# Kernel tuning notes

Hardware: AMD Instinct MI355X
Metric: run time of the kernel (lower is better)

Reference implementation:

```python
import jax, jax.numpy as jnp
import numpy as np

B, S, D, H = 4, 1024, 1024, 16
HD = D // H  # head_dim = 64
NEG = -1e9  # stands in for float('-inf') in masked_fill; numerically safe


def setup_inputs() -> dict:
    key = jax.random.key(0)
    ks = jax.random.split(key, 8)
    q = jax.random.normal(ks[0], (B, S, D), dtype=jnp.float32)
    k = jax.random.normal(ks[1], (B, S, D), dtype=jnp.float32)
    v = jax.random.normal(ks[2], (B, S, D), dtype=jnp.float32)
    # padding mask: True marks padded positions; pad out the tail of each sequence
    pos = jnp.arange(S)
    lengths = jnp.array([S, S - 64, S - 128, S - 256])
    padding_mask = pos[None, :] >= lengths[:, None]  # [B, S] bool
    # additive causal mask: 0 on/below diagonal, NEG above
    causal_mask = jnp.where(jnp.tril(jnp.ones((S, S), dtype=bool)), 0.0, NEG).astype(jnp.float32)
    scale = 1.0 / np.sqrt(D)
    Wq = jax.random.normal(ks[3], (D, D), dtype=jnp.float32) * scale
    Wk = jax.random.normal(ks[4], (D, D), dtype=jnp.float32) * scale
    Wv = jax.random.normal(ks[5], (D, D), dtype=jnp.float32) * scale
    Wo = jax.random.normal(ks[6], (D, D), dtype=jnp.float32) * scale
    return {"q": q, "k": k, "v": v, "padding_mask": padding_mask,
            "causal_mask": causal_mask, "Wq": Wq, "Wk": Wk, "Wv": Wv,
            "Wo": Wo, "n_heads": H}


def reference(q, k, v, padding_mask, causal_mask, Wq, Wk, Wv, Wo, n_heads):
    b, s, d = q.shape
    hd = d // n_heads
    # projections (nn.Linear: x @ W^T, no bias)
    qp = (q @ Wq.T).reshape(b, s, n_heads, hd).transpose(0, 2, 1, 3)  # [b,h,s,hd]
    kp = (k @ Wk.T).reshape(b, s, n_heads, hd).transpose(0, 2, 1, 3)
    vp = (v @ Wv.T).reshape(b, s, n_heads, hd).transpose(0, 2, 1, 3)
    scores = jnp.einsum('bhqd,bhkd->bhqk', qp, kp) / jnp.sqrt(jnp.float32(hd))
    # masked_fill(padding_mask, -inf): mask broadcast over heads and query dim
    scores = jnp.where(padding_mask[:, None, None, :], NEG, scores)
    scores = scores + causal_mask  # additive causal mask
    attn = jax.nn.softmax(scores, axis=-1)
    out = jnp.einsum('bhqk,bhkd->bhqd', attn, vp)
    out = out.transpose(0, 2, 1, 3).reshape(b, s, d)
    return out @ Wo.T
```

## Files before the change

### kernel.cpp

```cpp
#include <hip/hip_runtime.h>
#include <hip/hip_bf16.h>

#define BB 4
#define SS 1024
#define DD 1024
#define HH 16
#define HD 64
#define MM (BB*SS)


typedef __bf16 bf16x8 __attribute__((ext_vector_type(8)));
typedef __bf16 bf16x4 __attribute__((ext_vector_type(4)));
typedef float  f32x4  __attribute__((ext_vector_type(4)));

__global__ __launch_bounds__(256) void expand_mask(const void* __restrict__ pmraw,
                                                   float* __restrict__ madd,
                                                   int n)
{
    const unsigned char* bytes = (const unsigned char*)pmraw;
    __shared__ int isbool;
    if (threadIdx.x == 0) isbool = 0;
    __syncthreads();
    int flag = 0;
    for (int idx = threadIdx.x; idx < n; idx += 256) {
        if ((idx & 3) && bytes[idx]) flag = 1;
    }
    if (flag) atomicOr(&isbool, 1);
    __syncthreads();
    int i = blockIdx.x * 256 + threadIdx.x;
    if (i < n) {
        int v = isbool ? (int)bytes[i] : ((const int*)pmraw)[i];
        madd[i] = (v != 0) ? -1e9f : 0.0f;
    }
}

__global__ __launch_bounds__(256) void conv3(const float* __restrict__ s0,
                                             const float* __restrict__ s1,
                                             const float* __restrict__ s2,
                                             __bf16* __restrict__ d0,
                                             __bf16* __restrict__ d1,
                                             __bf16* __restrict__ d2)
{
    const float* s; __bf16* d;
    if (blockIdx.y == 0)      { s = s0; d = d0; }
    else if (blockIdx.y == 1) { s = s1; d = d1; }
    else                      { s = s2; d = d2; }
    int i = (blockIdx.x * 256 + threadIdx.x) * 4;
    float4 x = *(const float4*)(s + i);
    bf16x4 o;
    o[0] = (__bf16)x.x; o[1] = (__bf16)x.y;
    o[2] = (__bf16)x.z; o[3] = (__bf16)x.w;
    *(bf16x4*)(d + i) = o;
}

__global__ __launch_bounds__(256) void conv4(const float* __restrict__ s0,
                                             const float* __restrict__ s1,
                                             const float* __restrict__ s2,
                                             const float* __restrict__ s3,
                                             __bf16* __restrict__ d0,
                                             __bf16* __restrict__ d1,
                                             __bf16* __restrict__ d2,
                                             __bf16* __restrict__ d3)
{
    const float* s; __bf16* d;
    if (blockIdx.y == 0)      { s = s0; d = d0; }
    else if (blockIdx.y == 1) { s = s1; d = d1; }
    else if (blockIdx.y == 2) { s = s2; d = d2; }
    else                      { s = s3; d = d3; }
    int i = (blockIdx.x * 256 + threadIdx.x) * 4;
    float4 x = *(const float4*)(s + i);
    bf16x4 o;
    o[0] = (__bf16)x.x; o[1] = (__bf16)x.y;
    o[2] = (__bf16)x.z; o[3] = (__bf16)x.w;
    *(bf16x4*)(d + i) = o;
}

#define GM 128
#define GN 64
#define GK 64

__global__ __launch_bounds__(256) void gemm_qkv(const __bf16* __restrict__ qb,
                                                const __bf16* __restrict__ kb,
                                                const __bf16* __restrict__ vb,
                                                const __bf16* __restrict__ Wqb,
                                                const __bf16* __restrict__ Wkb,
                                                const __bf16* __restrict__ Wvb,
                                                __bf16* __restrict__ Qp,
                                                __bf16* __restrict__ Kp,
                                                __bf16* __restrict__ VpT)
{
    __shared__ __align__(16) __bf16 As[GM][GK];
    __shared__ __align__(16) __bf16 Bs[GN][GK];

    const __bf16 *A, *W; __bf16* C;
    const int z = blockIdx.z;
    if (z == 0)      { A = qb; W = Wqb; C = Qp;  }
    else if (z == 1) { A = kb; W = Wkb; C = Kp;  }
    else             { A = vb; W = Wvb; C = VpT; }

    const int tid  = threadIdx.x;
    const int lane = tid & 63;
    const int w    = tid >> 6;
    const int l15  = lane & 15;
    const int quad = lane >> 4;
    const int wr   = w >> 1;
    const int wc   = w & 1;

    const int m0 = blockIdx.y * GM;
    const int n0 = blockIdx.x * GN;

    const int srow = tid >> 3;
    const int scol = (tid & 7) * 8;

    const __bf16* gA = A + (size_t)(m0 + srow) * DD + scol;
    const __bf16* gB = W + (size_t)(n0 + srow) * DD + scol;

    f32x4 acc[4][2] = {};

    for (int k0 = 0; k0 < DD; k0 += GK) {
        __syncthreads();
        #pragma unroll
        for (int c = 0; c < 4; ++c)
            __builtin_amdgcn_global_load_lds(
                (const __attribute__((address_space(1))) void*)(gA + (size_t)c * 32 * DD + k0),
                (__attribute__((address_space(3))) void*)(&As[c * 32 + srow][scol]), 16, 0, 0);
        #pragma unroll
        for (int c = 0; c < 2; ++c)
            __builtin_amdgcn_global_load_lds(
                (const __attribute__((address_space(1))) void*)(gB + (size_t)c * 32 * DD + k0),
                (__attribute__((address_space(3))) void*)(&Bs[c * 32 + srow][scol]), 16, 0, 0);
        __syncthreads();

        #pragma unroll
        for (int ks = 0; ks < 2; ++ks) {
            bf16x8 af[4], bf[2];
            #pragma unroll
            for (int mt = 0; mt < 4; ++mt)
                af[mt] = *(const bf16x8*)&As[wr * 64 + mt * 16 + l15][ks * 32 + quad * 8];
            #pragma unroll
            for (int nt = 0; nt < 2; ++nt)
                bf[nt] = *(const bf16x8*)&Bs[wc * 32 + nt * 16 + l15][ks * 32 + quad * 8];
            #pragma unroll
            for (int mt = 0; mt < 4; ++mt)
                #pragma unroll
                for (int nt = 0; nt < 2; ++nt)
                    acc[mt][nt] = __builtin_amdgcn_mfma_f32_16x16x32_bf16(
                        af[mt], bf[nt], acc[mt][nt], 0, 0, 0);
        }
    }

    if (z == 0) {
        #pragma unroll
        for (int mt = 0; mt < 4; ++mt)
            #pragma unroll
            for (int nt = 0; nt < 2; ++nt)
                #pragma unroll
                for (int r = 0; r < 4; ++r)
                    acc[mt][nt][r] *= 0.125f;
    }

    if (z == 2) {
        #pragma unroll
        for (int mt = 0; mt < 4; ++mt)
            #pragma unroll
            for (int nt = 0; nt < 2; ++nt) {
                bf16x4 o;
                #pragma unroll
                for (int r = 0; r < 4; ++r) o[r] = (__bf16)acc[mt][nt][r];
                const int n = n0 + wc * 32 + nt * 16 + l15;
                const int m = m0 + wr * 64 + mt * 16 + quad * 4;
                *(bf16x4*)&C[(size_t)n * MM + m] = o;
            }
    } else {
        #pragma unroll
        for (int mt = 0; mt < 4; ++mt)
            #pragma unroll
            for (int nt = 0; nt < 2; ++nt)
                #pragma unroll
                for (int r = 0; r < 4; ++r)
                    C[(size_t)(m0 + wr * 64 + mt * 16 + quad * 4 + r) * DD +
                      (n0 + wc * 32 + nt * 16 + l15)] = (__bf16)acc[mt][nt][r];
    }
}

__global__ __launch_bounds__(256) void gemm_wo(const __bf16* __restrict__ A,
                                               const __bf16* __restrict__ W,
                                               float* __restrict__ C)
{
    __shared__ __align__(16) __bf16 As[64][64];
    __shared__ __align__(16) __bf16 Bs[64][64];

    const int tid  = threadIdx.x;
    const int lane = tid & 63;
    const int w    = tid >> 6;
    const int l15  = lane & 15;
    const int quad = lane >> 4;
    const int wr   = w >> 1;
    const int wc   = w & 1;

    const int m0 = blockIdx.y * 64;
    const int n0 = blockIdx.x * 64;

    const int srow = tid >> 3;
    const int scol = (tid & 7) * 8;

    const __bf16* gA = A + (size_t)(m0 + srow) * DD + scol;
    const __bf16* gB = W + (size_t)(n0 + srow) * DD + scol;

    f32x4 acc[2][2] = {};

    for (int k0 = 0; k0 < DD; k0 += 64) {
        __syncthreads();
        #pragma unroll
        for (int c = 0; c < 2; ++c)
            __builtin_amdgcn_global_load_lds(
                (const __attribute__((address_space(1))) void*)(gA + (size_t)c * 32 * DD + k0),
                (__attribute__((address_space(3))) void*)(&As[c * 32 + srow][scol]), 16, 0, 0);
        #pragma unroll
        for (int c = 0; c < 2; ++c)
            __builtin_amdgcn_global_load_lds(
                (const __attribute__((address_space(1))) void*)(gB + (size_t)c * 32 * DD + k0),
                (__attribute__((address_space(3))) void*)(&Bs[c * 32 + srow][scol]), 16, 0, 0);
        __syncthreads();

        #pragma unroll
        for (int ks = 0; ks < 2; ++ks) {
            bf16x8 af[2], bf[2];
            #pragma unroll
            for (int mt = 0; mt < 2; ++mt)
                af[mt] = *(const bf16x8*)&As[wr * 32 + mt * 16 + l15][ks * 32 + quad * 8];
            #pragma unroll
            for (int nt = 0; nt < 2; ++nt)
                bf[nt] = *(const bf16x8*)&Bs[wc * 32 + nt * 16 + l15][ks * 32 + quad * 8];
            #pragma unroll
            for (int mt = 0; mt < 2; ++mt)
                #pragma unroll
                for (int nt = 0; nt < 2; ++nt)
                    acc[mt][nt] = __builtin_amdgcn_mfma_f32_16x16x32_bf16(
                        af[mt], bf[nt], acc[mt][nt], 0, 0, 0);
        }
    }

    #pragma unroll
    for (int mt = 0; mt < 2; ++mt)
        #pragma unroll
        for (int nt = 0; nt < 2; ++nt)
            #pragma unroll
            for (int r = 0; r < 4; ++r)
                C[(size_t)(m0 + wr * 32 + mt * 16 + quad * 4 + r) * DD +
                  (n0 + wc * 32 + nt * 16 + l15)] = acc[mt][nt][r];
}

#define PSTRIDE 72

__global__ __launch_bounds__(256) void flash_attn(const __bf16* __restrict__ Qp,
                                                  const __bf16* __restrict__ Kp,
                                                  const __bf16* __restrict__ VpT,
                                                  const float* __restrict__ maskadd,
                                                  __bf16* __restrict__ Op)
{
    __shared__ __bf16 Pl[4][16][PSTRIDE];
    __shared__ float  Obuf[2][16][68];

    const int tid  = threadIdx.x;
    const int lane = tid & 63;
    const int w    = tid >> 6;
    const int l15  = lane & 15;
    const int quad = lane >> 4;
    const int h    = w & 1;
    const int tile = w >> 1;

    const int bh = blockIdx.x;
    const int hh = bh & (HH - 1);
    const int b  = bh >> 4;
    const int qt = tile ? (63 - (int)blockIdx.y) : (int)blockIdx.y;

    const size_t hbase = (size_t)b * SS * DD + (size_t)hh * HD;
    const int qrow0 = qt * 16;
    const int lastkt = qt >> 2;

    bf16x8 qf0, qf1;
    {
        const __bf16* qptr = Qp + hbase + (size_t)(qrow0 + l15) * DD + quad * 8;
        qf0 = *(const bf16x8*)(qptr);
        qf1 = *(const bf16x8*)(qptr + 32);
    }

    const __bf16* vt = VpT + (size_t)(hh * HD) * MM + b * SS;
    const float* madd = maskadd + b * SS;

    f32x4 Ov[4] = {};
    float lsum[4] = {};

    for (int kt = h; kt <= lastkt; kt += 2) {
        f32x4 Sv[4] = {};
        #pragma unroll
        for (int nt = 0; nt < 4; ++nt) {
            const __bf16* kptr = Kp + hbase +
                (size_t)(kt * 64 + nt * 16 + l15) * DD + quad * 8;
            bf16x8 kf0 = *(const bf16x8*)(kptr);
            bf16x8 kf1 = *(const bf16x8*)(kptr + 32);
            Sv[nt] = __builtin_amdgcn_mfma_f32_16x16x32_bf16(qf0, kf0, Sv[nt], 0, 0, 0);
            Sv[nt] = __builtin_amdgcn_mfma_f32_16x16x32_bf16(qf1, kf1, Sv[nt], 0, 0, 0);
        }

        #pragma unroll
        for (int nt = 0; nt < 4; ++nt) {
            const int j  = kt * 64 + nt * 16 + l15;
            const float ma = madd[j];
            #pragma unroll
            for (int r = 0; r < 4; ++r) {
                const int i = qrow0 + quad * 4 + r;
                float p = __expf(Sv[nt][r] + ma);
                if (j > i) p = 0.f;
                Sv[nt][r] = p;
                lsum[r] += p;
            }
        }

        #pragma unroll
        for (int nt = 0; nt < 4; ++nt)
            #pragma unroll
            for (int r = 0; r < 4; ++r)
                Pl[w][quad * 4 + r][nt * 16 + l15] = (__bf16)Sv[nt][r];

        bf16x8 pf0 = *(const bf16x8*)&Pl[w][l15][quad * 8];
        bf16x8 pf1 = *(const bf16x8*)&Pl[w][l15][quad * 8 + 32];

        #pragma unroll
        for (int dt = 0; dt < 4; ++dt) {
            const __bf16* vptr = vt + (size_t)(dt * 16 + l15) * MM + kt * 64 + quad * 8;
            bf16x8 vf0 = *(const bf16x8*)(vptr);
            bf16x8 vf1 = *(const bf16x8*)(vptr + 32);
            Ov[dt] = __builtin_amdgcn_mfma_f32_16x16x32_bf16(pf0, vf0, Ov[dt], 0, 0, 0);
            Ov[dt] = __builtin_amdgcn_mfma_f32_16x16x32_bf16(pf1, vf1, Ov[dt], 0, 0, 0);
        }
    }

    #pragma unroll
    for (int off = 1; off < 16; off <<= 1)
        #pragma unroll
        for (int r = 0; r < 4; ++r)
            lsum[r] += __shfl_xor(lsum[r], off);

    if (h == 1) {
        #pragma unroll
        for (int dt = 0; dt < 4; ++dt)
            #pragma unroll
            for (int r = 0; r < 4; ++r)
                Obuf[tile][quad * 4 + r][dt * 16 + l15] = Ov[dt][r];
        if (l15 == 0)
            #pragma unroll
            for (int r = 0; r < 4; ++r)
                Obuf[tile][quad * 4 + r][64] = lsum[r];
    }
    __syncthreads();
    if (h == 0) {
        float rcp[4];
        #pragma unroll
        for (int r = 0; r < 4; ++r)
            rcp[r] = 1.0f / (lsum[r] + Obuf[tile][quad * 4 + r][64]);
        #pragma unroll
        for (int dt = 0; dt < 4; ++dt)
            #pragma unroll
            for (int r = 0; r < 4; ++r) {
                const int i = qrow0 + quad * 4 + r;
                float o = Ov[dt][r] + Obuf[tile][quad * 4 + r][dt * 16 + l15];
                Op[hbase + (size_t)i * DD + dt * 16 + l15] = (__bf16)(o * rcp[r]);
            }
    }
}

extern "C" void kernel_launch(void* const* d_in, const int* in_sizes, int n_in,
                              void* d_out, int out_size, void* d_ws, size_t ws_size,
                              hipStream_t stream)
{
    const float* q  = (const float*)d_in[0];
    const float* k  = (const float*)d_in[1];
    const float* v  = (const float*)d_in[2];
    const void*  pm = d_in[3];
    const float* Wq = (const float*)d_in[5];
    const float* Wk = (const float*)d_in[6];
    const float* Wv = (const float*)d_in[7];
    const float* Wo = (const float*)d_in[8];

    char* ws = (char*)d_ws;
    float* madd = (float*)ws;
    const size_t MB = 1024 * 1024;
    char* base = ws + 65536;

    __bf16* qb  = (__bf16*)(base +  0 * MB);
    __bf16* kb  = (__bf16*)(base +  8 * MB);
    __bf16* vb  = (__bf16*)(base + 16 * MB);
    __bf16* Wqb = (__bf16*)(base + 24 * MB);
    __bf16* Wkb = (__bf16*)(base + 26 * MB);
    __bf16* Wvb = (__bf16*)(base + 28 * MB);
    __bf16* Wob = (__bf16*)(base + 30 * MB);
    __bf16* Qp  = (__bf16*)(base + 32 * MB);
    __bf16* Kp  = (__bf16*)(base + 40 * MB);
    __bf16* VpT = (__bf16*)(base + 48 * MB);
    __bf16* Op  = qb;

    float* out = (float*)d_out;
    const int NT = MM * DD;
    const int NW = DD * DD;

    expand_mask<<<(BB * SS) / 256, 256, 0, stream>>>(pm, madd, BB * SS);
    conv3<<<dim3(NT / 1024, 3), 256, 0, stream>>>(q, k, v, qb, kb, vb);
    conv4<<<dim3(NW / 1024, 4), 256, 0, stream>>>(Wq, Wk, Wv, Wo, Wqb, Wkb, Wvb, Wob);

    dim3 gg(DD / GN, MM / GM, 3);
    gemm_qkv<<<gg, 256, 0, stream>>>(qb, kb, vb, Wqb, Wkb, Wvb, Qp, Kp, VpT);

    dim3 ga(BB * HH, 32);
    flash_attn<<<ga, 256, 0, stream>>>(Qp, Kp, VpT, madd, Op);

    dim3 gw(DD / 64, MM / 64);
    gemm_wo<<<gw, 256, 0, stream>>>(Op, Wob, out);
}
```

Measured before the change: 256.8 us.

## Enlarge flash-attention query tile to 64 rows per wave for K/V reuse

Each wave now processes 64 query rows (four 16-row sub-tiles) instead of 16, so every K and V fragment loaded from global memory feeds four times as many MFMAs. Scores are computed transposed (K as the A operand), which lets the mask be read as float4 and P be written to LDS as bf16x4. The causal check is applied only on the diagonal block, and shared memory is aliased between the P and O buffers. The grid shrinks from 32 to 8 blocks per head, and register pressure rises from 64 accumulators plus Q and P fragments, which may lower occupancy and parallelism.

```diff
diff --git a/kernel.cpp b/kernel.cpp
--- a/kernel.cpp
+++ b/kernel.cpp
@@ -251,16 +251,18 @@
                   (n0 + wc * 32 + nt * 16 + l15)] = acc[mt][nt][r];
 }
 
-#define PSTRIDE 72
-
-__global__ __launch_bounds__(256) void flash_attn(const __bf16* __restrict__ Qp,
-                                                  const __bf16* __restrict__ Kp,
-                                                  const __bf16* __restrict__ VpT,
-                                                  const float* __restrict__ maskadd,
-                                                  __bf16* __restrict__ Op)
-{
-    __shared__ __bf16 Pl[4][16][PSTRIDE];
-    __shared__ float  Obuf[2][16][68];
+#define PSTR 72
+#define OSTR 68
+
+__global__ __launch_bounds__(256, 2) void flash_attn(const __bf16* __restrict__ Qp,
+                                                     const __bf16* __restrict__ Kp,
+                                                     const __bf16* __restrict__ VpT,
+                                                     const float* __restrict__ maskadd,
+                                                     __bf16* __restrict__ Op)
+{
+    __shared__ __align__(16) unsigned char smem[4 * 64 * PSTR * 2];
+    __bf16 (*Pl)[64][PSTR]  = (__bf16 (*)[64][PSTR])smem;
+    float  (*Obuf)[64][OSTR] = (float (*)[64][OSTR])smem;
 
     const int tid  = threadIdx.x;
     const int lane = tid & 63;
@@ -273,101 +275,121 @@
     const int bh = blockIdx.x;
     const int hh = bh & (HH - 1);
     const int b  = bh >> 4;
-    const int qt = tile ? (63 - (int)blockIdx.y) : (int)blockIdx.y;
+    const int p  = blockIdx.y;
+    const int m  = tile ? (15 - p) : p;
 
     const size_t hbase = (size_t)b * SS * DD + (size_t)hh * HD;
-    const int qrow0 = qt * 16;
-    const int lastkt = qt >> 2;
-
-    bf16x8 qf0, qf1;
-    {
-        const __bf16* qptr = Qp + hbase + (size_t)(qrow0 + l15) * DD + quad * 8;
-        qf0 = *(const bf16x8*)(qptr);
-        qf1 = *(const bf16x8*)(qptr + 32);
+    const int q0 = m * 64;
+
+    bf16x8 qf[4][2];
+    #pragma unroll
+    for (int qt = 0; qt < 4; ++qt) {
+        const __bf16* qp = Qp + hbase + (size_t)(q0 + qt * 16 + l15) * DD + quad * 8;
+        qf[qt][0] = *(const bf16x8*)qp;
+        qf[qt][1] = *(const bf16x8*)(qp + 32);
     }
 
     const __bf16* vt = VpT + (size_t)(hh * HD) * MM + b * SS;
     const float* madd = maskadd + b * SS;
 
-    f32x4 Ov[4] = {};
-    float lsum[4] = {};
-
-    for (int kt = h; kt <= lastkt; kt += 2) {
-        f32x4 Sv[4] = {};
-        #pragma unroll
-        for (int nt = 0; nt < 4; ++nt) {
-            const __bf16* kptr = Kp + hbase +
-                (size_t)(kt * 64 + nt * 16 + l15) * DD + quad * 8;
-            bf16x8 kf0 = *(const bf16x8*)(kptr);
-            bf16x8 kf1 = *(const bf16x8*)(kptr + 32);
-            Sv[nt] = __builtin_amdgcn_mfma_f32_16x16x32_bf16(qf0, kf0, Sv[nt], 0, 0, 0);
-            Sv[nt] = __builtin_amdgcn_mfma_f32_16x16x32_bf16(qf1, kf1, Sv[nt], 0, 0, 0);
-        }
-
-        #pragma unroll
-        for (int nt = 0; nt < 4; ++nt) {
-            const int j  = kt * 64 + nt * 16 + l15;
-            const float ma = madd[j];
-            #pragma unroll
-            for (int r = 0; r < 4; ++r) {
-                const int i = qrow0 + quad * 4 + r;
-                float p = __expf(Sv[nt][r] + ma);
-                if (j > i) p = 0.f;
-                Sv[nt][r] = p;
-                lsum[r] += p;
+    f32x4 Ov[4][4] = {};
+    float lsumq[4] = {};
+
+    for (int kt = h; kt <= m; kt += 2) {
+        const int kbase = kt * 64;
+        const bool diag = (kt == m);
+
+        f32x4 St[4][4];
+        #pragma unroll
+        for (int kg = 0; kg < 4; ++kg) {
+            const __bf16* kp = Kp + hbase + (size_t)(kbase + kg * 16 + l15) * DD + quad * 8;
+            bf16x8 kf0 = *(const bf16x8*)kp;
+            bf16x8 kf1 = *(const bf16x8*)(kp + 32);
+            #pragma unroll
+            for (int qt = 0; qt < 4; ++qt) {
+                f32x4 s = {};
+                s = __builtin_amdgcn_mfma_f32_16x16x32_bf16(kf0, qf[qt][0], s, 0, 0, 0);
+                s = __builtin_amdgcn_mfma_f32_16x16x32_bf16(kf1, qf[qt][1], s, 0, 0, 0);
+                St[kg][qt] = s;
             }
         }
 
         #pragma unroll
-        for (int nt = 0; nt < 4; ++nt)
-            #pragma unroll
-            for (int r = 0; r < 4; ++r)
-                Pl[w][quad * 4 + r][nt * 16 + l15] = (__bf16)Sv[nt][r];
-
-        bf16x8 pf0 = *(const bf16x8*)&Pl[w][l15][quad * 8];
-        bf16x8 pf1 = *(const bf16x8*)&Pl[w][l15][quad * 8 + 32];
+        for (int kg = 0; kg < 4; ++kg) {
+            const float4 mr = *(const float4*)&madd[kbase + kg * 16 + quad * 4];
+            #pragma unroll
+            for (int qt = 0; qt < 4; ++qt) {
+                const int i = q0 + qt * 16 + l15;
+                bf16x4 pk;
+                #pragma unroll
+                for (int r = 0; r < 4; ++r) {
+                    const int j = kbase + kg * 16 + quad * 4 + r;
+                    float pv = __expf(St[kg][qt][r] + ((const float*)&mr)[r]);
+                    if (diag && j > i) pv = 0.f;
+                    lsumq[qt] += pv;
+                    pk[r] = (__bf16)pv;
+                }
+                *(bf16x4*)&Pl[w][qt * 16 + l15][kg * 16 + quad * 4] = pk;
+            }
+        }
+
+        bf16x8 pf[4][2];
+        #pragma unroll
+        for (int qt = 0; qt < 4; ++qt) {
+            pf[qt][0] = *(const bf16x8*)&Pl[w][qt * 16 + l15][quad * 8];
+            pf[qt][1] = *(const bf16x8*)&Pl[w][qt * 16 + l15][quad * 8 + 32];
+        }
 
         #pragma unroll
         for (int dt = 0; dt < 4; ++dt) {
-            const __bf16* vptr = vt + (size_t)(dt * 16 + l15) * MM + kt * 64 + quad * 8;
-            bf16x8 vf0 = *(const bf16x8*)(vptr);
-            bf16x8 vf1 = *(const bf16x8*)(vptr + 32);
-            Ov[dt] = __builtin_amdgcn_mfma_f32_16x16x32_bf16(pf0, vf0, Ov[dt], 0, 0, 0);
-            Ov[dt] = __builtin_amdgcn_mfma_f32_16x16x32_bf16(pf1, vf1, Ov[dt], 0, 0, 0);
+            const __bf16* vp = vt + (size_t)(dt * 16 + l15) * MM + kbase + quad * 8;
+            bf16x8 vf0 = *(const bf16x8*)vp;
+            bf16x8 vf1 = *(const bf16x8*)(vp + 32);
+            #pragma unroll
+            for (int qt = 0; qt < 4; ++qt) {
+                Ov[qt][dt] = __builtin_amdgcn_mfma_f32_16x16x32_bf16(pf[qt][0], vf0, Ov[qt][dt], 0, 0, 0);
+                Ov[qt][dt] = __builtin_amdgcn_mfma_f32_16x16x32_bf16(pf[qt][1], vf1, Ov[qt][dt], 0, 0, 0);
+            }
         }
     }
 
     #pragma unroll
-    for (int off = 1; off < 16; off <<= 1)
-        #pragma unroll
-        for (int r = 0; r < 4; ++r)
-            lsum[r] += __shfl_xor(lsum[r], off);
-
+    for (int off = 16; off < 64; off <<= 1)
+        #pragma unroll
+        for (int qt = 0; qt < 4; ++qt)
+            lsumq[qt] += __shfl_xor(lsumq[qt], off);
+
+    __syncthreads();
     if (h == 1) {
         #pragma unroll
-        for (int dt = 0; dt < 4; ++dt)
-            #pragma unroll
-            for (int r = 0; r < 4; ++r)
-                Obuf[tile][quad * 4 + r][dt * 16 + l15] = Ov[dt][r];
-        if (l15 == 0)
-            #pragma unroll
-            for (int r = 0; r < 4; ++r)
-                Obuf[tile][quad * 4 + r][64] = lsum[r];
+        for (int qt = 0; qt < 4; ++qt) {
+            #pragma unroll
+            for (int dt = 0; dt < 4; ++dt)
+                #pragma unroll
+                for (int r = 0; r < 4; ++r)
+                    Obuf[tile][qt * 16 + quad * 4 + r][dt * 16 + l15] = Ov[qt][dt][r];
+            if (quad == 0)
+                Obuf[tile][qt * 16 + l15][64] = lsumq[qt];
+        }
     }
     __syncthreads();
     if (h == 0) {
-        float rcp[4];
-        #pragma unroll
-        for (int r = 0; r < 4; ++r)
-            rcp[r] = 1.0f / (lsum[r] + Obuf[tile][quad * 4 + r][64]);
-        #pragma unroll
-        for (int dt = 0; dt < 4; ++dt)
-            #pragma unroll
-            for (int r = 0; r < 4; ++r) {
-                const int i = qrow0 + quad * 4 + r;
-                float o = Ov[dt][r] + Obuf[tile][quad * 4 + r][dt * 16 + l15];
-                Op[hbase + (size_t)i * DD + dt * 16 + l15] = (__bf16)(o * rcp[r]);
-            }
+        #pragma unroll
+        for (int qt = 0; qt < 4; ++qt) {
+            const float rcp = 1.0f / (lsumq[qt] + Obuf[tile][qt * 16 + l15][64]);
+            float rq[4];
+            #pragma unroll
+            for (int r = 0; r < 4; ++r) rq[r] = __shfl(rcp, quad * 4 + r);
+            #pragma unroll
+            for (int dt = 0; dt < 4; ++dt)
+                #pragma unroll
+                for (int r = 0; r < 4; ++r) {
+                    const int i = q0 + qt * 16 + quad * 4 + r;
+                    float o = Ov[qt][dt][r] +
+                              Obuf[tile][qt * 16 + quad * 4 + r][dt * 16 + l15];
+                    Op[hbase + (size_t)i * DD + dt * 16 + l15] = (__bf16)(o * rq[r]);
+                }
+        }
     }
 }
 
@@ -412,7 +434,7 @@
     dim3 gg(DD / GN, MM / GM, 3);
     gemm_qkv<<<gg, 256, 0, stream>>>(qb, kb, vb, Wqb, Wkb, Wvb, Qp, Kp, VpT);
 
-    dim3 ga(BB * HH, 32);
+    dim3 ga(BB * HH, 8);
     flash_attn<<<ga, 256, 0, stream>>>(Qp, Kp, VpT, madd, Op);
 
     dim3 gw(DD / 64, MM / 64);
```

Result: faster. 230.2 us (-10.4%).
